# Optimization experiments

Measured on AMD Instinct MI355X. Metric: run time of the kernel, lower is better.

Reference implementation:

```python
import jax, jax.numpy as jnp
import numpy as np

B = 128            # number of subgraphs (one head, one tail each)
NODES_PER_G = 64
N = B * NODES_PER_G  # 8192 total nodes
E = 131072           # total edges in the batched graph
NUM_RELS = 200
D = 64               # rel_emb_dim
EMB = 64             # emb_dim
L = 3                # num_gcn_layers (jumping-knowledge concat)
REPR = L * EMB       # 192, g.ndata['repr'] feature width
LINK_MODE = 6


def setup_inputs() -> dict:
    key = jax.random.key(0)
    ks = jax.random.split(key, 10)
    node_repr = jax.random.normal(ks[0], (N, REPR), jnp.float32)
    edge_src = jax.random.randint(ks[1], (E,), 0, N, dtype=jnp.int32)
    edge_dst = jax.random.randint(ks[2], (E,), 0, N, dtype=jnp.int32)
    edge_type = jax.random.randint(ks[3], (E,), 0, NUM_RELS, dtype=jnp.int32)
    rel_labels = jax.random.randint(ks[4], (B,), 0, NUM_RELS, dtype=jnp.int32)
    node_graph_id = (jnp.arange(N) // NODES_PER_G).astype(jnp.int32)
    head_ids = (jnp.arange(B) * NODES_PER_G).astype(jnp.int32)   # node with id==1 per graph
    tail_ids = head_ids + 1                                      # node with id==2 per graph
    rel_emb_w = jax.random.normal(ks[5], (NUM_RELS, D), jnp.float32)
    W_reld = jax.random.normal(ks[6], (LINK_MODE, D, D), jnp.float32) * 0.05
    b_reld = jnp.zeros((LINK_MODE, D), jnp.float32)
    Wc = jax.random.normal(ks[7], (D, 2 * D), jnp.float32) * 0.05
    bc = jnp.zeros((D,), jnp.float32)
    Wf = jax.random.normal(ks[8], (1, 3 * REPR + D), jnp.float32) * 0.05
    bf = jnp.zeros((1,), jnp.float32)
    return {
        'node_repr': node_repr, 'rel_emb_w': rel_emb_w, 'W_reld': W_reld,
        'b_reld': b_reld, 'Wc': Wc, 'bc': bc, 'Wf': Wf, 'bf': bf,
        'edge_src': edge_src, 'edge_dst': edge_dst, 'edge_type': edge_type,
        'rel_labels': rel_labels, 'node_graph_id': node_graph_id,
        'head_ids': head_ids, 'tail_ids': tail_ids,
    }


def reference(node_repr, rel_emb_w, W_reld, b_reld, Wc, bc, Wf, bf,
              edge_src, edge_dst, edge_type, rel_labels, node_graph_id,
              head_ids, tail_ids):
    f32 = jnp.float32
    nb = head_ids.shape[0]
    # Six edge connection modes, [B, E] each (row b selects edges incident to
    # the head/tail node of subgraph b).
    io = (edge_dst[None, :] == head_ids[:, None]).astype(f32)  # in_edge_out
    oo = (edge_src[None, :] == head_ids[:, None]).astype(f32)  # out_edge_out
    ii = (edge_dst[None, :] == tail_ids[:, None]).astype(f32)  # in_edge_in
    oi = (edge_src[None, :] == tail_ids[:, None]).astype(f32)  # out_edge_in
    m5 = oo * ii   # edge_mode_5: head -> tail edges
    m6 = io * oi   # edge_mode_6: tail -> head edges
    modes = jnp.stack([io - m6, oo - m5, ii - m5, oi - m6, m5, m6])  # [6,B,E]
    norms = modes.sum(-1, keepdims=True) + 1e-30                      # [6,B,1]
    # Per-mode linear transform of relation embeddings, then aggregate.
    rel_feat = rel_emb_w[edge_type]                                   # [E,D]
    trans = jnp.einsum('ed,mfd->mef', rel_feat, W_reld) + b_reld[:, None, :]  # [6,E,D]
    contrib = jnp.einsum('mbe,med->mbd', modes, trans) / norms        # [6,B,D]
    rel_neighbor = contrib.mean(0)                                    # sum(...)/link_mode
    rel_final = jnp.concatenate([rel_neighbor, rel_emb_w[rel_labels]], -1) @ Wc.T + bc
    rel_final = jax.nn.relu(rel_final)
    rel_final = rel_final / jnp.maximum(
        jnp.linalg.norm(rel_final, axis=-1, keepdims=True), 1e-12)
    # mean_nodes(g, 'repr') per subgraph
    g_sum = jax.ops.segment_sum(node_repr, node_graph_id, num_segments=nb)
    counts = jax.ops.segment_sum(jnp.ones((node_repr.shape[0],), f32),
                                 node_graph_id, num_segments=nb)
    g_out = g_sum / counts[:, None]
    g_rep = jnp.concatenate(
        [g_out, node_repr[head_ids], node_repr[tail_ids], rel_final], -1)
    return g_rep @ Wf.T + bf   # [B, 1]
```

## Files before the change

kernel.cpp:

```cpp
#include <hip/hip_runtime.h>

#define NGRAPH 128
#define NEDGE  131072
#define DIM    64
#define REPRW  192
#define LISTCAP 1024


__global__ __launch_bounds__(256) void edge_scan_kernel(
    const int* __restrict__ esrc, const int* __restrict__ edst,
    const int* __restrict__ etype, int* __restrict__ gcnt,
    int* __restrict__ glist)
{
    const int i = blockIdx.x * 256 + threadIdx.x;
    const int4 ss = ((const int4*)esrc)[i];
    const int4 dd = ((const int4*)edst)[i];
    #pragma unroll
    for (int c = 0; c < 4; c++) {
        const int s = (c == 0) ? ss.x : (c == 1) ? ss.y : (c == 2) ? ss.z : ss.w;
        const int d = (c == 0) ? dd.x : (c == 1) ? dd.y : (c == 2) ? dd.z : dd.w;
        const bool hs = (s & 63) < 2;
        const bool hd = (d & 63) < 2;
        if (hd | hs) {
            const int et = etype[4 * i + c];
            if (hd) {
                const int g = d >> 6, gb = g << 6;
                int m = -1;
                if (d == gb)       m = (s == gb + 1) ? 5 : 0;
                else if (s != gb)  m = 2;
                if (m >= 0) {
                    int slot = atomicAdd(&gcnt[g], 1);
                    if (slot < LISTCAP) glist[g * LISTCAP + slot] = (m << 8) | et;
                }
            }
            if (hs) {
                const int g = s >> 6, gb = g << 6;
                int m = -1;
                if (s == gb)       m = (d == gb + 1) ? 4 : 1;
                else if (d != gb)  m = 3;
                if (m >= 0) {
                    int slot = atomicAdd(&gcnt[g], 1);
                    if (slot < LISTCAP) glist[g * LISTCAP + slot] = (m << 8) | et;
                }
            }
        }
    }
}

__global__ __launch_bounds__(1024) void graph_finish_kernel(
    const float* __restrict__ node_repr, const float* __restrict__ rel_emb,
    const float* __restrict__ W_reld, const float* __restrict__ b_reld,
    const float* __restrict__ Wc, const float* __restrict__ bc,
    const float* __restrict__ Wf, const float* __restrict__ bf,
    const int* __restrict__ rel_labels,
    const int* __restrict__ head_ids, const int* __restrict__ tail_ids,
    const int* __restrict__ gcnt, const int* __restrict__ glist,
    float* __restrict__ out)
{
    const int b    = blockIdx.x;
    const int tid  = threadIdx.x;
    const int base = b << 6;
    const int wave = tid >> 6;
    const int lane = tid & 63;

    __shared__ __align__(16) float shS[6 * 64];
    __shared__ float shCnt[6];
    __shared__ int   shNH;
    __shared__ float sh_grep[640];
    __shared__ float sh_part[4 * 192];
    __shared__ float sh_v[6 * 64];
    __shared__ float sh_rn[64];
    __shared__ float sh_Wc[64 * 129];
    __shared__ float sh_red[16];

    if (tid < 384) shS[tid] = 0.0f;
    if (tid < 6)   shCnt[tid] = 0.0f;
    if (tid == 0) {
        int n = gcnt[b];
        shNH = n < LISTCAP ? n : LISTCAP;
    }
    __syncthreads();

    {
        const int nh = shNH;
        const int* mylist = glist + b * LISTCAP;
        for (int h = wave; h < nh; h += 16) {
            int ent = mylist[h];
            int m = ent >> 8, t = ent & 0xff;
            atomicAdd(&shS[m * 64 + lane], rel_emb[t * 64 + lane]);
            if (lane == 0) atomicAdd(&shCnt[m], 1.0f);
        }
    }
    {
        int r = tid / 192, col = tid - r * 192;
        if (tid < 768) {
            const float* p = node_repr + (size_t)(base + r * 16) * REPRW + col;
            float a = 0.0f;
            #pragma unroll
            for (int n = 0; n < 16; n++) a += p[(size_t)n * REPRW];
            sh_part[r * 192 + col] = a;
        }
        if (tid < 192) {
            sh_grep[192 + tid] = node_repr[(size_t)head_ids[b] * REPRW + tid];
            sh_grep[384 + tid] = node_repr[(size_t)tail_ids[b] * REPRW + tid];
        }
    }
    __syncthreads();

    if (tid < 384) {
        int m = wave, f = lane;
        const float4* Wrow = (const float4*)(W_reld + (m * 64 + f) * 64);
        const float4* Sv   = (const float4*)(shS + m * 64);
        float dot = 0.0f;
        #pragma unroll
        for (int k = 0; k < 16; k++) {
            float4 w = Wrow[k];
            float4 sv = Sv[k];
            dot += w.x * sv.x + w.y * sv.y + w.z * sv.z + w.w * sv.w;
        }
        float cm = shCnt[m];
        sh_v[m * 64 + f] = (dot + cm * b_reld[m * 64 + f]) / (cm + 1e-30f);
    } else {
        for (int j = tid - 384; j < 64 * 128; j += 1024 - 384) {
            int row = j >> 7, col = j & 127;
            sh_Wc[row * 129 + col] = Wc[j];
        }
    }
    __syncthreads();

    if (tid < 64) {
        sh_rn[tid] = (sh_v[tid] + sh_v[64 + tid] + sh_v[128 + tid] +
                      sh_v[192 + tid] + sh_v[256 + tid] + sh_v[320 + tid]) * (1.0f / 6.0f);
    } else if (tid >= 128 && tid < 320) {
        int j = tid - 128;
        sh_grep[j] = (sh_part[j] + sh_part[192 + j] +
                      sh_part[384 + j] + sh_part[576 + j]) * (1.0f / 64.0f);
    }
    __syncthreads();

    if (tid < 64) {
        const float* rl = rel_emb + rel_labels[b] * DIM;
        const float* Wrow = sh_Wc + tid * 129;
        float z = bc[tid];
        #pragma unroll 8
        for (int j = 0; j < 64; j++) z += sh_rn[j] * Wrow[j];
        #pragma unroll 8
        for (int j = 0; j < 64; j++) z += rl[j] * Wrow[64 + j];
        z = fmaxf(z, 0.0f);
        float sq = z * z;
        #pragma unroll
        for (int off = 32; off >= 1; off >>= 1) sq += __shfl_xor(sq, off);
        float nrm = fmaxf(sqrtf(sq), 1e-12f);
        sh_grep[576 + tid] = z / nrm;
    }
    __syncthreads();

    if (tid < 640) {
        float p = sh_grep[tid] * Wf[tid];
        #pragma unroll
        for (int off = 32; off >= 1; off >>= 1) p += __shfl_xor(p, off);
        if (lane == 0) sh_red[wave] = p;
    }
    __syncthreads();
    if (tid == 0) {
        float acc = bf[0];
        #pragma unroll
        for (int w = 0; w < 10; w++) acc += sh_red[w];
        out[b] = acc;
    }
}

extern "C" void kernel_launch(void* const* d_in, const int* in_sizes, int n_in,
                              void* d_out, int out_size, void* d_ws, size_t ws_size,
                              hipStream_t stream) {
    (void)in_sizes; (void)n_in; (void)out_size; (void)ws_size;

    const float* node_repr = (const float*)d_in[0];
    const float* rel_emb   = (const float*)d_in[1];
    const float* W_reld    = (const float*)d_in[2];
    const float* b_reld    = (const float*)d_in[3];
    const float* Wc        = (const float*)d_in[4];
    const float* bc        = (const float*)d_in[5];
    const float* Wf        = (const float*)d_in[6];
    const float* bf        = (const float*)d_in[7];
    const int*   esrc      = (const int*)d_in[8];
    const int*   edst      = (const int*)d_in[9];
    const int*   etype     = (const int*)d_in[10];
    const int*   rel_labels= (const int*)d_in[11];
    const int*   head_ids  = (const int*)d_in[13];
    const int*   tail_ids  = (const int*)d_in[14];

    int* gcnt  = (int*)d_ws;
    int* glist = (int*)((char*)d_ws + 512);

    hipMemsetAsync(gcnt, 0, NGRAPH * sizeof(int), stream);
    edge_scan_kernel<<<NEDGE / 4 / 256, 256, 0, stream>>>(
        esrc, edst, etype, gcnt, glist);
    graph_finish_kernel<<<NGRAPH, 1024, 0, stream>>>(
        node_repr, rel_emb, W_reld, b_reld, Wc, bc, Wf, bf,
        rel_labels, head_ids, tail_ids, gcnt, glist, (float*)d_out);
}
```

Baseline: 118.4 us.

## Fuse edge scan and graph finish into one cooperative kernel with grid syncs

Replaces the memset plus two kernel launches with a single cooperative launch of 128 blocks of 1024 threads. The counter zeroing, the edge scan (one edge per thread, 1024 edges per block) and the per-graph finish stage are separated by grid-wide syncs. The node-mean partial sums are computed before the first sync so they overlap with it. This removes launch overhead and the gaps between kernels, but adds two grid barriers and scans edges with scalar instead of int4 loads.

```diff
diff --git a/kernel.cpp b/kernel.cpp
--- a/kernel.cpp
+++ b/kernel.cpp
@@ -1,60 +1,25 @@
 #include <hip/hip_runtime.h>
+#include <hip/hip_cooperative_groups.h>
+
+namespace cg = cooperative_groups;
 
 #define NGRAPH 128
 #define NEDGE  131072
 #define DIM    64
 #define REPRW  192
+#define NTHREADS 1024
 #define LISTCAP 1024
-
-
-__global__ __launch_bounds__(256) void edge_scan_kernel(
-    const int* __restrict__ esrc, const int* __restrict__ edst,
-    const int* __restrict__ etype, int* __restrict__ gcnt,
-    int* __restrict__ glist)
-{
-    const int i = blockIdx.x * 256 + threadIdx.x;
-    const int4 ss = ((const int4*)esrc)[i];
-    const int4 dd = ((const int4*)edst)[i];
-    #pragma unroll
-    for (int c = 0; c < 4; c++) {
-        const int s = (c == 0) ? ss.x : (c == 1) ? ss.y : (c == 2) ? ss.z : ss.w;
-        const int d = (c == 0) ? dd.x : (c == 1) ? dd.y : (c == 2) ? dd.z : dd.w;
-        const bool hs = (s & 63) < 2;
-        const bool hd = (d & 63) < 2;
-        if (hd | hs) {
-            const int et = etype[4 * i + c];
-            if (hd) {
-                const int g = d >> 6, gb = g << 6;
-                int m = -1;
-                if (d == gb)       m = (s == gb + 1) ? 5 : 0;
-                else if (s != gb)  m = 2;
-                if (m >= 0) {
-                    int slot = atomicAdd(&gcnt[g], 1);
-                    if (slot < LISTCAP) glist[g * LISTCAP + slot] = (m << 8) | et;
-                }
-            }
-            if (hs) {
-                const int g = s >> 6, gb = g << 6;
-                int m = -1;
-                if (s == gb)       m = (d == gb + 1) ? 4 : 1;
-                else if (d != gb)  m = 3;
-                if (m >= 0) {
-                    int slot = atomicAdd(&gcnt[g], 1);
-                    if (slot < LISTCAP) glist[g * LISTCAP + slot] = (m << 8) | et;
-                }
-            }
-        }
-    }
-}
-
-__global__ __launch_bounds__(1024) void graph_finish_kernel(
+#define EPB (NEDGE / NGRAPH)
+
+__global__ __launch_bounds__(NTHREADS) void fused_graph_kernel(
     const float* __restrict__ node_repr, const float* __restrict__ rel_emb,
     const float* __restrict__ W_reld, const float* __restrict__ b_reld,
     const float* __restrict__ Wc, const float* __restrict__ bc,
     const float* __restrict__ Wf, const float* __restrict__ bf,
-    const int* __restrict__ rel_labels,
+    const int* __restrict__ esrc, const int* __restrict__ edst,
+    const int* __restrict__ etype, const int* __restrict__ rel_labels,
     const int* __restrict__ head_ids, const int* __restrict__ tail_ids,
-    const int* __restrict__ gcnt, const int* __restrict__ glist,
+    int* __restrict__ gcnt, int* __restrict__ glist,
     float* __restrict__ out)
 {
     const int b    = blockIdx.x;
@@ -65,7 +30,6 @@
 
     __shared__ __align__(16) float shS[6 * 64];
     __shared__ float shCnt[6];
-    __shared__ int   shNH;
     __shared__ float sh_grep[640];
     __shared__ float sh_part[4 * 192];
     __shared__ float sh_v[6 * 64];
@@ -75,22 +39,8 @@
 
     if (tid < 384) shS[tid] = 0.0f;
     if (tid < 6)   shCnt[tid] = 0.0f;
-    if (tid == 0) {
-        int n = gcnt[b];
-        shNH = n < LISTCAP ? n : LISTCAP;
-    }
-    __syncthreads();
-
-    {
-        const int nh = shNH;
-        const int* mylist = glist + b * LISTCAP;
-        for (int h = wave; h < nh; h += 16) {
-            int ent = mylist[h];
-            int m = ent >> 8, t = ent & 0xff;
-            atomicAdd(&shS[m * 64 + lane], rel_emb[t * 64 + lane]);
-            if (lane == 0) atomicAdd(&shCnt[m], 1.0f);
-        }
-    }
+    if (tid == 0)  atomicExch(&gcnt[b], 0);
+
     {
         int r = tid / 192, col = tid - r * 192;
         if (tid < 768) {
@@ -105,6 +55,54 @@
             sh_grep[384 + tid] = node_repr[(size_t)tail_ids[b] * REPRW + tid];
         }
     }
+
+    cg::this_grid().sync();
+
+    {
+        const int e = b * EPB + tid;
+        const int s = esrc[e];
+        const int d = edst[e];
+        const bool hd = (d & 63) < 2;
+        const bool hs = (s & 63) < 2;
+        if (hd | hs) {
+            const int et = etype[e];
+            if (hd) {
+                const int g = d >> 6, gb = g << 6;
+                int m = (d == gb) ? ((s == gb + 1) ? 5 : 0)
+                                  : ((s == gb) ? -1 : 2);
+                if (m >= 0) {
+                    int slot = atomicAdd(&gcnt[g], 1);
+                    if (slot < LISTCAP) glist[g * LISTCAP + slot] = (m << 8) | et;
+                }
+            }
+            if (hs) {
+                const int g = s >> 6, gb = g << 6;
+                int m = (s == gb) ? ((d == gb + 1) ? 4 : 1)
+                                  : ((d == gb) ? -1 : 3);
+                if (m >= 0) {
+                    int slot = atomicAdd(&gcnt[g], 1);
+                    if (slot < LISTCAP) glist[g * LISTCAP + slot] = (m << 8) | et;
+                }
+            }
+        }
+    }
+    __threadfence();
+    cg::this_grid().sync();
+
+    {
+        int nh = gcnt[b];
+        if (nh > LISTCAP) nh = LISTCAP;
+        const int* mylist = glist + b * LISTCAP;
+        for (int h = wave; h < nh; h += 16) {
+            int ent = mylist[h];
+            int m = ent >> 8, t = ent & 0xff;
+            atomicAdd(&shS[m * 64 + lane], rel_emb[t * 64 + lane]);
+            if (lane == 0) atomicAdd(&shCnt[m], 1.0f);
+        }
+        if (tid < 192)
+            sh_grep[tid] = (sh_part[tid] + sh_part[192 + tid] +
+                            sh_part[384 + tid] + sh_part[576 + tid]) * (1.0f / 64.0f);
+    }
     __syncthreads();
 
     if (tid < 384) {
@@ -121,7 +119,7 @@
         float cm = shCnt[m];
         sh_v[m * 64 + f] = (dot + cm * b_reld[m * 64 + f]) / (cm + 1e-30f);
     } else {
-        for (int j = tid - 384; j < 64 * 128; j += 1024 - 384) {
+        for (int j = tid - 384; j < 64 * 128; j += NTHREADS - 384) {
             int row = j >> 7, col = j & 127;
             sh_Wc[row * 129 + col] = Wc[j];
         }
@@ -131,10 +129,6 @@
     if (tid < 64) {
         sh_rn[tid] = (sh_v[tid] + sh_v[64 + tid] + sh_v[128 + tid] +
                       sh_v[192 + tid] + sh_v[256 + tid] + sh_v[320 + tid]) * (1.0f / 6.0f);
-    } else if (tid >= 128 && tid < 320) {
-        int j = tid - 128;
-        sh_grep[j] = (sh_part[j] + sh_part[192 + j] +
-                      sh_part[384 + j] + sh_part[576 + j]) * (1.0f / 64.0f);
     }
     __syncthreads();
 
@@ -192,11 +186,15 @@
 
     int* gcnt  = (int*)d_ws;
     int* glist = (int*)((char*)d_ws + 512);
-
-    hipMemsetAsync(gcnt, 0, NGRAPH * sizeof(int), stream);
-    edge_scan_kernel<<<NEDGE / 4 / 256, 256, 0, stream>>>(
-        esrc, edst, etype, gcnt, glist);
-    graph_finish_kernel<<<NGRAPH, 1024, 0, stream>>>(
-        node_repr, rel_emb, W_reld, b_reld, Wc, bc, Wf, bf,
-        rel_labels, head_ids, tail_ids, gcnt, glist, (float*)d_out);
+    float* outp = (float*)d_out;
+
+    void* args[] = {
+        (void*)&node_repr, (void*)&rel_emb, (void*)&W_reld, (void*)&b_reld,
+        (void*)&Wc, (void*)&bc, (void*)&Wf, (void*)&bf,
+        (void*)&esrc, (void*)&edst, (void*)&etype, (void*)&rel_labels,
+        (void*)&head_ids, (void*)&tail_ids,
+        (void*)&gcnt, (void*)&glist, (void*)&outp
+    };
+    hipLaunchCooperativeKernel((const void*)fused_graph_kernel,
+                               dim3(NGRAPH), dim3(NTHREADS), args, 0, stream);
 }
```

Result: slower. 206.3 us (+74.3%).
